# Kernel optimization log

Hardware: AMD Instinct MI355X
Metric: run time of the kernel (lower is better)

Reference implementation:

```python
import jax, jax.numpy as jnp
import numpy as np

HEADS = 8
DIM_HEAD = 32
DIM = HEADS * DIM_HEAD  # 256
B, H, W = 2, 256, 256


def _dw2d(x, wgt):
    # depthwise 3x3 conv, NCHW, weight (C,1,3,3)
    return jax.lax.conv_general_dilated(
        x, wgt, window_strides=(1, 1), padding='SAME',
        feature_group_count=x.shape[1],
        dimension_numbers=('NCHW', 'OIHW', 'NCHW'))


def setup_inputs() -> dict:
    key = jax.random.key(0)
    ks = jax.random.split(key, 20)
    def kaiming(k, shape, fan_in):
        return jax.random.normal(k, shape, jnp.float32) * np.sqrt(2.0 / fan_in)
    inp = {}
    inp['x_in'] = jax.random.normal(ks[0], (B, H, W, DIM), jnp.float32)
    # shared depthwise weights (heads,1,3,3), kaiming_normal fan_in=9
    names = ['qw1', 'qw2', 'qw3', 'kw1', 'kw2', 'kw3', 'vw1', 'vw2', 'vw3']
    for i, n in enumerate(names):
        inp[n] = kaiming(ks[1 + i], (HEADS, 1, 3, 3), 9)
    # pos_emb: two depthwise convs dim->dim with bias
    inp['pos_w1'] = kaiming(ks[10], (DIM, 1, 3, 3), 9)
    inp['pos_b1'] = jnp.zeros((DIM,), jnp.float32)
    inp['pos_w2'] = kaiming(ks[11], (DIM, 1, 3, 3), 9)
    inp['pos_b2'] = jnp.zeros((DIM,), jnp.float32)
    # conv1d heads->heads kernel 3
    inp['conv1d_w'] = kaiming(ks[12], (HEADS, HEADS, 3), HEADS * 3)
    inp['conv1d_b'] = jnp.zeros((HEADS,), jnp.float32)
    inp['rescale'] = jnp.ones((HEADS, 1, 1), jnp.float32)
    inp['rescale2'] = jnp.ones((HEADS, 1, 1), jnp.float32)
    inp['proj_w'] = kaiming(ks[13], (DIM, DIM), DIM)  # (out,in) torch layout
    inp['proj_b'] = jnp.zeros((DIM,), jnp.float32)
    return inp


def reference(x_in, qw1, qw2, qw3, kw1, kw2, kw3, vw1, vw2, vw3,
              pos_w1, pos_b1, pos_w2, pos_b2, conv1d_w, conv1d_b,
              rescale, rescale2, proj_w, proj_b):
    b, h, w, c = x_in.shape
    heads = rescale.shape[0]
    dim_head = c // heads
    x = jnp.transpose(x_in, (0, 3, 1, 2))  # NCHW
    # positional embedding: dwconv -> gelu(exact) -> dwconv
    t = _dw2d(x, pos_w1) + pos_b1[None, :, None, None]
    t = jax.nn.gelu(t, approximate=False)
    t = _dw2d(t, pos_w2) + pos_b2[None, :, None, None]
    x = x + t

    def chain(x, w1, w2, w3):
        for wgt in (w1, w2, w3):
            x = _dw2d(x, jnp.repeat(wgt, dim_head, axis=0))
        return x

    q = chain(x, qw1, qw2, qw3)
    k = chain(x, kw1, kw2, kw3)
    v = chain(x, vw1, vw2, vw3)
    # (b,c,h,w) -> (b,heads,dim_head,hw) ; channel = head*dim_head + d
    q = q.reshape(b, heads, dim_head, h * w)
    k = k.reshape(b, heads, dim_head, h * w)
    v = v.reshape(b, heads, dim_head, h * w)
    eps = 1e-12
    q = q / jnp.maximum(jnp.linalg.norm(q, axis=-1, keepdims=True), eps)
    k = k / jnp.maximum(jnp.linalg.norm(k, axis=-1, keepdims=True), eps)
    # channel attention: k @ q^T -> (b,heads,dim_head,dim_head)
    attn = jnp.einsum('bhdn,bhen->bhde', k, q)
    # pooled v -> conv1d over dim_head length, channels = heads
    y = v.mean(axis=-1)  # (b,heads,dim_head)
    attn_v = jax.lax.conv_general_dilated(
        y, conv1d_w, window_strides=(1,), padding='SAME',
        dimension_numbers=('NCH', 'OIH', 'NCH')) + conv1d_b[None, :, None]
    diag = attn_v[..., :, None] * jnp.eye(dim_head, dtype=attn.dtype)
    attn = attn * rescale[None] + diag * rescale2[None]
    attn = jax.nn.softmax(attn, axis=-1)
    out = jnp.einsum('bhde,bhen->bhdn', attn, v)  # (b,heads,dim_head,hw)
    out = jnp.transpose(out, (0, 3, 1, 2)).reshape(b, h * w, c)
    out = out @ proj_w.T + proj_b
    return out.reshape(b, h, w, c)
```

## Files before the change

### kernel.cpp

```cpp
#include <hip/hip_runtime.h>
#include <stdint.h>
#include <math.h>


using u16 = unsigned short;
using u32 = unsigned int;

typedef __bf16 bf16x8_t __attribute__((ext_vector_type(8)));
typedef float f32x4_t __attribute__((ext_vector_type(4)));

__device__ __forceinline__ float bf2f(u16 v) {
  u32 u = ((u32)v) << 16;
  return __builtin_bit_cast(float, u);
}
__device__ __forceinline__ u16 f2bf(float f) {
  u32 u = __builtin_bit_cast(u32, f);
  u32 r = u + 0x7fffu + ((u >> 16) & 1u);
  return (u16)(r >> 16);
}
__device__ __forceinline__ void unpack8(uint4 u, float f[8]) {
  f[0] = bf2f((u16)(u.x & 0xffffu)); f[1] = bf2f((u16)(u.x >> 16));
  f[2] = bf2f((u16)(u.y & 0xffffu)); f[3] = bf2f((u16)(u.y >> 16));
  f[4] = bf2f((u16)(u.z & 0xffffu)); f[5] = bf2f((u16)(u.z >> 16));
  f[6] = bf2f((u16)(u.w & 0xffffu)); f[7] = bf2f((u16)(u.w >> 16));
}
__device__ __forceinline__ uint4 pack8(const u16 o[8]) {
  uint4 v;
  v.x = (u32)o[0] | ((u32)o[1] << 16);
  v.y = (u32)o[2] | ((u32)o[3] << 16);
  v.z = (u32)o[4] | ((u32)o[5] << 16);
  v.w = (u32)o[6] | ((u32)o[7] << 16);
  return v;
}

__global__ __launch_bounds__(64) void compose_kernel(
    const float* __restrict__ qw1, const float* __restrict__ qw2,
    const float* __restrict__ qw3, const float* __restrict__ kw1,
    const float* __restrict__ kw2, const float* __restrict__ kw3,
    const float* __restrict__ vw1, const float* __restrict__ vw2,
    const float* __restrict__ vw3, float* __restrict__ Wc) {
  const int t = threadIdx.x;
  if (t >= 24) return;
  const int h = t / 3, c = t % 3;
  const float* w1 = (c == 0 ? qw1 : c == 1 ? kw1 : vw1) + h * 9;
  const float* w2 = (c == 0 ? qw2 : c == 1 ? kw2 : vw2) + h * 9;
  const float* w3 = (c == 0 ? qw3 : c == 1 ? kw3 : vw3) + h * 9;
  float w12[25];
  for (int i = 0; i < 25; ++i) w12[i] = 0.f;
  for (int ky = 0; ky < 3; ++ky)
    for (int kx = 0; kx < 3; ++kx)
      for (int ly = 0; ly < 3; ++ly)
        for (int lx = 0; lx < 3; ++lx)
          w12[(ky + ly) * 5 + kx + lx] += w2[ky * 3 + kx] * w1[ly * 3 + lx];
  float we[49];
  for (int i = 0; i < 49; ++i) we[i] = 0.f;
  for (int my = 0; my < 3; ++my)
    for (int mx = 0; mx < 3; ++mx)
      for (int ey = 0; ey < 5; ++ey)
        for (int ex = 0; ex < 5; ++ex)
          we[(my + ey) * 7 + mx + ex] += w3[my * 3 + mx] * w12[ey * 5 + ex];
  float* dst = Wc + (h * 3 + c) * 49;
  for (int i = 0; i < 49; ++i) dst[i] = we[i];
}

__global__ __launch_bounds__(256) void posemb_kernel(
    const float* __restrict__ xin, u16* __restrict__ x2,
    const float* __restrict__ w1g, const float* __restrict__ b1g,
    const float* __restrict__ w2g, const float* __restrict__ b2g) {
  const int t = threadIdx.x;
  const int o = t & 3;
  const int bz = blockIdx.z;
  const int cg = bz & 7;
  const int b = bz >> 3;
  const int x0 = blockIdx.x * 16;
  const int y0 = blockIdx.y * 8;
  const int c0 = cg * 32 + o * 8;

  __shared__ __align__(16) u16 Abuf[240 * 32];
  __shared__ __align__(16) u16 Bbuf[180 * 32];

  for (int i = t; i < 240 * 4; i += 256) {
    const int px = i >> 2, oo = i & 3;
    const int lx = px % 20, ly = px / 20;
    const int gx = x0 - 2 + lx, gy = y0 - 2 + ly;
    u16 ov[8];
    if (gx >= 0 && gx < 256 && gy >= 0 && gy < 256) {
      const float* p = xin + ((size_t)((b << 16) + (gy << 8) + gx)) * 256 + cg * 32 + oo * 8;
      const float4 r0 = *reinterpret_cast<const float4*>(p);
      const float4 r1 = *reinterpret_cast<const float4*>(p + 4);
      ov[0] = f2bf(r0.x); ov[1] = f2bf(r0.y); ov[2] = f2bf(r0.z); ov[3] = f2bf(r0.w);
      ov[4] = f2bf(r1.x); ov[5] = f2bf(r1.y); ov[6] = f2bf(r1.z); ov[7] = f2bf(r1.w);
    } else {
#pragma unroll
      for (int j = 0; j < 8; ++j) ov[j] = 0;
    }
    *reinterpret_cast<uint4*>(Abuf + px * 32 + oo * 8) = pack8(ov);
  }
  __syncthreads();

  {
    float w[72], bi[8];
#pragma unroll
    for (int j = 0; j < 8; ++j) {
#pragma unroll
      for (int k = 0; k < 9; ++k) w[j * 9 + k] = w1g[(c0 + j) * 9 + k];
      bi[j] = b1g[c0 + j];
    }
    for (int i = t; i < 180 * 4; i += 256) {
      const int px = i >> 2;
      const int sx = px % 18, sy = px / 18;
      const int gx = x0 - 1 + sx, gy = y0 - 1 + sy;
      const bool inb = (gx >= 0 && gx < 256 && gy >= 0 && gy < 256);
      float a[8];
#pragma unroll
      for (int j = 0; j < 8; ++j) a[j] = bi[j];
#pragma unroll
      for (int ky = 0; ky < 3; ++ky)
#pragma unroll
        for (int kx = 0; kx < 3; ++kx) {
          float f[8];
          unpack8(*reinterpret_cast<const uint4*>(
                      Abuf + ((sy + ky) * 20 + sx + kx) * 32 + o * 8), f);
#pragma unroll
          for (int j = 0; j < 8; ++j) a[j] = fmaf(w[j * 9 + ky * 3 + kx], f[j], a[j]);
        }
      u16 ov[8];
#pragma unroll
      for (int j = 0; j < 8; ++j) {
        const float g = 0.5f * a[j] * (1.0f + erff(a[j] * 0.70710678118654752f));
        ov[j] = inb ? f2bf(g) : (u16)0;
      }
      *reinterpret_cast<uint4*>(Bbuf + px * 32 + o * 8) = pack8(ov);
    }
  }
  __syncthreads();

  {
    float w[72], bi[8];
#pragma unroll
    for (int j = 0; j < 8; ++j) {
#pragma unroll
      for (int k = 0; k < 9; ++k) w[j * 9 + k] = w2g[(c0 + j) * 9 + k];
      bi[j] = b2g[c0 + j];
    }
    for (int i = t; i < 128 * 4; i += 256) {
      const int px = i >> 2;
      const int sx = px & 15, sy = px >> 4;
      float a[8];
#pragma unroll
      for (int j = 0; j < 8; ++j) a[j] = bi[j];
#pragma unroll
      for (int ky = 0; ky < 3; ++ky)
#pragma unroll
        for (int kx = 0; kx < 3; ++kx) {
          float f[8];
          unpack8(*reinterpret_cast<const uint4*>(
                      Bbuf + ((sy + ky) * 18 + sx + kx) * 32 + o * 8), f);
#pragma unroll
          for (int j = 0; j < 8; ++j) a[j] = fmaf(w[j * 9 + ky * 3 + kx], f[j], a[j]);
        }
      float xr[8];
      unpack8(*reinterpret_cast<const uint4*>(
                  Abuf + ((sy + 2) * 20 + sx + 2) * 32 + o * 8), xr);
      u16 ov[8];
#pragma unroll
      for (int j = 0; j < 8; ++j) ov[j] = f2bf(a[j] + xr[j]);
      u16* dst = x2 + ((size_t)((b << 16) + ((y0 + sy) << 8) + x0 + sx)) * 256 + cg * 32 + o * 8;
      *reinterpret_cast<uint4*>(dst) = pack8(ov);
    }
  }
}

__global__ __launch_bounds__(256) void qkv_fused_kernel(
    const u16* __restrict__ x2, u16* __restrict__ v3out,
    const float* __restrict__ Wc, float* __restrict__ G,
    float* __restrict__ sqq, float* __restrict__ sqk,
    float* __restrict__ vsum) {
  const int t = threadIdx.x;
  const int o = t & 3;
  const int sx = (t >> 2) & 15;
  const int yg = t >> 6;
  const int bz = blockIdx.z;
  const int h = bz & 7;
  const int b = bz >> 3;
  const int x0 = (blockIdx.x + 1) * 16;
  const int y0 = (blockIdx.y + 1) * 8;

  __shared__ __align__(16) u16 Abuf[308 * 32];
  __shared__ float rbuf[96];
  if (t < 96) rbuf[t] = 0.f;

  for (int i = t; i < 308 * 4; i += 256) {
    const int px = i >> 2, oo = i & 3;
    const int lx = px % 22, ly = px / 22;
    const int gx = x0 - 3 + lx, gy = y0 - 3 + ly;
    *reinterpret_cast<uint4*>(Abuf + px * 32 + oo * 8) =
        *reinterpret_cast<const uint4*>(
            x2 + ((size_t)((b << 16) + (gy << 8) + gx)) * 256 + h * 32 + oo * 8);
  }
  __syncthreads();

  const float* Wq = Wc + (h * 3 + 0) * 49;
  const float* Wk = Wc + (h * 3 + 1) * 49;
  const float* Wv = Wc + (h * 3 + 2) * 49;

  float aq[2][8], ak[2][8], av2[2][8];
#pragma unroll
  for (int r = 0; r < 2; ++r)
#pragma unroll
    for (int j = 0; j < 8; ++j) { aq[r][j] = 0.f; ak[r][j] = 0.f; av2[r][j] = 0.f; }

  const int ty0 = yg * 2;
  const u16* Arow0 = Abuf + (ty0 * 22 + sx) * 32 + o * 8;

  {
    const u16* Ar = Arow0;
#pragma unroll
    for (int jx = 0; jx < 7; ++jx) {
      float f[8];
      unpack8(*reinterpret_cast<const uint4*>(Ar + jx * 32), f);
      const float wq = Wq[jx], wk = Wk[jx], wv = Wv[jx];
#pragma unroll
      for (int j = 0; j < 8; ++j) {
        aq[0][j] = fmaf(wq, f[j], aq[0][j]);
        ak[0][j] = fmaf(wk, f[j], ak[0][j]);
        av2[0][j] = fmaf(wv, f[j], av2[0][j]);
      }
    }
  }
#pragma unroll 1
  for (int iy = 1; iy <= 6; ++iy) {
    const u16* Ar = Arow0 + iy * (22 * 32);
    const float* wq0 = Wq + iy * 7;
    const float* wk0 = Wk + iy * 7;
    const float* wv0 = Wv + iy * 7;
#pragma unroll
    for (int jx = 0; jx < 7; ++jx) {
      float f[8];
      unpack8(*reinterpret_cast<const uint4*>(Ar + jx * 32), f);
      float w;
      w = wq0[jx];
#pragma unroll
      for (int j = 0; j < 8; ++j) aq[0][j] = fmaf(w, f[j], aq[0][j]);
      w = wq0[jx - 7];
#pragma unroll
      for (int j = 0; j < 8; ++j) aq[1][j] = fmaf(w, f[j], aq[1][j]);
      w = wk0[jx];
#pragma unroll
      for (int j = 0; j < 8; ++j) ak[0][j] = fmaf(w, f[j], ak[0][j]);
      w = wk0[jx - 7];
#pragma unroll
      for (int j = 0; j < 8; ++j) ak[1][j] = fmaf(w, f[j], ak[1][j]);
      w = wv0[jx];
#pragma unroll
      for (int j = 0; j < 8; ++j) av2[0][j] = fmaf(w, f[j], av2[0][j]);
      w = wv0[jx - 7];
#pragma unroll
      for (int j = 0; j < 8; ++j) av2[1][j] = fmaf(w, f[j], av2[1][j]);
    }
  }
  {
    const u16* Ar = Arow0 + 7 * (22 * 32);
#pragma unroll
    for (int jx = 0; jx < 7; ++jx) {
      float f[8];
      unpack8(*reinterpret_cast<const uint4*>(Ar + jx * 32), f);
      const float wq = Wq[42 + jx], wk = Wk[42 + jx], wv = Wv[42 + jx];
#pragma unroll
      for (int j = 0; j < 8; ++j) {
        aq[1][j] = fmaf(wq, f[j], aq[1][j]);
        ak[1][j] = fmaf(wk, f[j], ak[1][j]);
        av2[1][j] = fmaf(wv, f[j], av2[1][j]);
      }
    }
  }

  __syncthreads();

  u16* K3s = Abuf;
  u16* Q3s = Abuf + 32 * 132;

  float rq[8], rk[8], rv[8];
#pragma unroll
  for (int j = 0; j < 8; ++j) { rq[j] = 0.f; rk[j] = 0.f; rv[j] = 0.f; }
#pragma unroll
  for (int ry = 0; ry < 2; ++ry) {
    const int px = (ty0 + ry) * 16 + sx;
    u16 ov[8];
#pragma unroll
    for (int j = 0; j < 8; ++j) {
      const u16 qb = f2bf(aq[ry][j]);
      Q3s[(o * 8 + j) * 132 + px] = qb;
      const float qf = bf2f(qb);
      rq[j] = fmaf(qf, qf, rq[j]);
      const u16 kb = f2bf(ak[ry][j]);
      K3s[(o * 8 + j) * 132 + px] = kb;
      const float kf = bf2f(kb);
      rk[j] = fmaf(kf, kf, rk[j]);
      ov[j] = f2bf(av2[ry][j]);
      rv[j] += bf2f(ov[j]);
    }
    u16* dst = v3out + ((size_t)((b << 16) + ((y0 + ty0 + ry) << 8) + x0 + sx)) * 256 + h * 32 + o * 8;
    *reinterpret_cast<uint4*>(dst) = pack8(ov);
  }
#pragma unroll
  for (int j = 0; j < 8; ++j) {
    atomicAdd(&rbuf[o * 8 + j], rq[j]);
    atomicAdd(&rbuf[32 + o * 8 + j], rk[j]);
    atomicAdd(&rbuf[64 + o * 8 + j], rv[j]);
  }
  __syncthreads();

  const int wave = t >> 6;
  const int lane = t & 63;
  const int quad = lane >> 4;
  const int l15 = lane & 15;
  const int d0 = (wave & 1) * 16;
  const int e0 = (wave >> 1) * 16;
  f32x4_t acc = {0.f, 0.f, 0.f, 0.f};
#pragma unroll
  for (int kb = 0; kb < 4; ++kb) {
    const bf16x8_t avf = *reinterpret_cast<const bf16x8_t*>(
        &K3s[(d0 + l15) * 132 + kb * 32 + quad * 8]);
    const bf16x8_t bvf = *reinterpret_cast<const bf16x8_t*>(
        &Q3s[(e0 + l15) * 132 + kb * 32 + quad * 8]);
    acc = __builtin_amdgcn_mfma_f32_16x16x32_bf16(avf, bvf, acc, 0, 0, 0);
  }
  float* Gp = G + (size_t)((b * 8 + h) * 32) * 32;
#pragma unroll
  for (int r = 0; r < 4; ++r)
    atomicAdd(&Gp[(d0 + quad * 4 + r) * 32 + e0 + l15], acc[r]);

  if (t < 32) atomicAdd(&sqq[b * 256 + h * 32 + t], rbuf[t]);
  else if (t < 64) atomicAdd(&sqk[b * 256 + h * 32 + (t - 32)], rbuf[t]);
  else if (t < 96) atomicAdd(&vsum[b * 256 + h * 32 + (t - 64)], rbuf[t]);
}

__device__ __forceinline__ void border_map(int bi, int& bx, int& by) {
  if (bi < 16) { bx = bi; by = 0; }
  else if (bi < 32) { bx = bi - 16; by = 31; }
  else { const int e = bi - 32; by = 1 + (e >> 1); bx = (e & 1) * 15; }
}

template <int RED, int BORDER>
__global__ __launch_bounds__(256) void chain3_kernel(
    const u16* __restrict__ in, u16* __restrict__ out,
    const float* __restrict__ w1g, const float* __restrict__ w2g,
    const float* __restrict__ w3g, float* __restrict__ red) {
  const int t = threadIdx.x;
  const int o = t & 3;
  const int bz = blockIdx.z;
  const int h = bz & 7;
  const int b = bz >> 3;
  int bx = blockIdx.x, by = blockIdx.y;
  if (BORDER) border_map(blockIdx.x, bx, by);
  const int x0 = bx * 16;
  const int y0 = by * 8;

  __shared__ __align__(16) u16 Abuf[308 * 32];
  __shared__ __align__(16) u16 Bbuf[240 * 32];
  __shared__ float rbuf[32];
  if (t < 32) rbuf[t] = 0.f;

  float w1[9], w2[9], w3[9];
#pragma unroll
  for (int k = 0; k < 9; ++k) {
    w1[k] = w1g[h * 9 + k];
    w2[k] = w2g[h * 9 + k];
    w3[k] = w3g[h * 9 + k];
  }

  for (int i = t; i < 308 * 4; i += 256) {
    const int px = i >> 2, oo = i & 3;
    const int lx = px % 22, ly = px / 22;
    const int gx = x0 - 3 + lx, gy = y0 - 3 + ly;
    uint4 v = {0, 0, 0, 0};
    if (gx >= 0 && gx < 256 && gy >= 0 && gy < 256)
      v = *reinterpret_cast<const uint4*>(
          in + ((size_t)((b << 16) + (gy << 8) + gx)) * 256 + h * 32 + oo * 8);
    *reinterpret_cast<uint4*>(Abuf + px * 32 + oo * 8) = v;
  }
  __syncthreads();

  for (int i = t; i < 240 * 4; i += 256) {
    const int px = i >> 2;
    const int sx = px % 20, sy = px / 20;
    const int gx = x0 - 2 + sx, gy = y0 - 2 + sy;
    const bool inb = (gx >= 0 && gx < 256 && gy >= 0 && gy < 256);
    float a[8] = {0, 0, 0, 0, 0, 0, 0, 0};
#pragma unroll
    for (int ky = 0; ky < 3; ++ky)
#pragma unroll
      for (int kx = 0; kx < 3; ++kx) {
        float f[8];
        unpack8(*reinterpret_cast<const uint4*>(
                    Abuf + ((sy + ky) * 22 + sx + kx) * 32 + o * 8), f);
#pragma unroll
        for (int j = 0; j < 8; ++j) a[j] = fmaf(w1[ky * 3 + kx], f[j], a[j]);
      }
    u16 ov[8];
#pragma unroll
    for (int j = 0; j < 8; ++j) ov[j] = inb ? f2bf(a[j]) : (u16)0;
    *reinterpret_cast<uint4*>(Bbuf + px * 32 + o * 8) = pack8(ov);
  }
  __syncthreads();

  for (int i = t; i < 180 * 4; i += 256) {
    const int px = i >> 2;
    const int sx = px % 18, sy = px / 18;
    const int gx = x0 - 1 + sx, gy = y0 - 1 + sy;
    const bool inb = (gx >= 0 && gx < 256 && gy >= 0 && gy < 256);
    float a[8] = {0, 0, 0, 0, 0, 0, 0, 0};
#pragma unroll
    for (int ky = 0; ky < 3; ++ky)
#pragma unroll
      for (int kx = 0; kx < 3; ++kx) {
        float f[8];
        unpack8(*reinterpret_cast<const uint4*>(
                    Bbuf + ((sy + ky) * 20 + sx + kx) * 32 + o * 8), f);
#pragma unroll
        for (int j = 0; j < 8; ++j) a[j] = fmaf(w2[ky * 3 + kx], f[j], a[j]);
      }
    u16 ov[8];
#pragma unroll
    for (int j = 0; j < 8; ++j) ov[j] = inb ? f2bf(a[j]) : (u16)0;
    *reinterpret_cast<uint4*>(Abuf + px * 32 + o * 8) = pack8(ov);
  }
  __syncthreads();

  float racc[8] = {0, 0, 0, 0, 0, 0, 0, 0};
  for (int i = t; i < 128 * 4; i += 256) {
    const int px = i >> 2;
    const int sx = px & 15, sy = px >> 4;
    float a[8] = {0, 0, 0, 0, 0, 0, 0, 0};
#pragma unroll
    for (int ky = 0; ky < 3; ++ky)
#pragma unroll
      for (int kx = 0; kx < 3; ++kx) {
        float f[8];
        unpack8(*reinterpret_cast<const uint4*>(
                    Abuf + ((sy + ky) * 18 + sx + kx) * 32 + o * 8), f);
#pragma unroll
        for (int j = 0; j < 8; ++j) a[j] = fmaf(w3[ky * 3 + kx], f[j], a[j]);
      }
    u16 ov[8];
#pragma unroll
    for (int j = 0; j < 8; ++j) {
      ov[j] = f2bf(a[j]);
      const float rv = bf2f(ov[j]);
      if (RED == 1) racc[j] = fmaf(rv, rv, racc[j]);
      if (RED == 2) racc[j] += rv;
    }
    u16* dst = out + ((size_t)((b << 16) + ((y0 + sy) << 8) + x0 + sx)) * 256 + h * 32 + o * 8;
    *reinterpret_cast<uint4*>(dst) = pack8(ov);
  }
  __syncthreads();
#pragma unroll
  for (int j = 0; j < 8; ++j) atomicAdd(&rbuf[o * 8 + j], racc[j]);
  __syncthreads();
  if (t < 32) atomicAdd(&red[b * 256 + h * 32 + t], rbuf[t]);
}

template <int BORDER>
__global__ __launch_bounds__(256) void kchain_gram_kernel(
    const u16* __restrict__ in, const u16* __restrict__ q3,
    const float* __restrict__ w1g, const float* __restrict__ w2g,
    const float* __restrict__ w3g, float* __restrict__ G, float* __restrict__ sqk) {
  const int t = threadIdx.x;
  const int o = t & 3;
  const int bz = blockIdx.z;
  const int h = bz & 7;
  const int b = bz >> 3;
  int bx = blockIdx.x, by = blockIdx.y;
  if (BORDER) border_map(blockIdx.x, bx, by);
  const int x0 = bx * 16;
  const int y0 = by * 8;

  __shared__ __align__(16) u16 Abuf[308 * 32];
  __shared__ __align__(16) u16 Bbuf[240 * 32];
  __shared__ __align__(16) u16 K3s[32 * 132];
  __shared__ __align__(16) u16 Q3s[32 * 132];
  __shared__ float rbuf[32];
  if (t < 32) rbuf[t] = 0.f;

  float w1[9], w2[9], w3[9];
#pragma unroll
  for (int k = 0; k < 9; ++k) {
    w1[k] = w1g[h * 9 + k];
    w2[k] = w2g[h * 9 + k];
    w3[k] = w3g[h * 9 + k];
  }

  for (int i = t; i < 308 * 4; i += 256) {
    const int px = i >> 2, oo = i & 3;
    const int lx = px % 22, ly = px / 22;
    const int gx = x0 - 3 + lx, gy = y0 - 3 + ly;
    uint4 v = {0, 0, 0, 0};
    if (gx >= 0 && gx < 256 && gy >= 0 && gy < 256)
      v = *reinterpret_cast<const uint4*>(
          in + ((size_t)((b << 16) + (gy << 8) + gx)) * 256 + h * 32 + oo * 8);
    *reinterpret_cast<uint4*>(Abuf + px * 32 + oo * 8) = v;
  }
  __syncthreads();

  for (int i = t; i < 240 * 4; i += 256) {
    const int px = i >> 2;
    const int sx = px % 20, sy = px / 20;
    const int gx = x0 - 2 + sx, gy = y0 - 2 + sy;
    const bool inb = (gx >= 0 && gx < 256 && gy >= 0 && gy < 256);
    float a[8] = {0, 0, 0, 0, 0, 0, 0, 0};
#pragma unroll
    for (int ky = 0; ky < 3; ++ky)
#pragma unroll
      for (int kx = 0; kx < 3; ++kx) {
        float f[8];
        unpack8(*reinterpret_cast<const uint4*>(
                    Abuf + ((sy + ky) * 22 + sx + kx) * 32 + o * 8), f);
#pragma unroll
        for (int j = 0; j < 8; ++j) a[j] = fmaf(w1[ky * 3 + kx], f[j], a[j]);
      }
    u16 ov[8];
#pragma unroll
    for (int j = 0; j < 8; ++j) ov[j] = inb ? f2bf(a[j]) : (u16)0;
    *reinterpret_cast<uint4*>(Bbuf + px * 32 + o * 8) = pack8(ov);
  }
  __syncthreads();

  for (int i = t; i < 180 * 4; i += 256) {
    const int px = i >> 2;
    const int sx = px % 18, sy = px / 18;
    const int gx = x0 - 1 + sx, gy = y0 - 1 + sy;
    const bool inb = (gx >= 0 && gx < 256 && gy >= 0 && gy < 256);
    float a[8] = {0, 0, 0, 0, 0, 0, 0, 0};
#pragma unroll
    for (int ky = 0; ky < 3; ++ky)
#pragma unroll
      for (int kx = 0; kx < 3; ++kx) {
        float f[8];
        unpack8(*reinterpret_cast<const uint4*>(
                    Bbuf + ((sy + ky) * 20 + sx + kx) * 32 + o * 8), f);
#pragma unroll
        for (int j = 0; j < 8; ++j) a[j] = fmaf(w2[ky * 3 + kx], f[j], a[j]);
      }
    u16 ov[8];
#pragma unroll
    for (int j = 0; j < 8; ++j) ov[j] = inb ? f2bf(a[j]) : (u16)0;
    *reinterpret_cast<uint4*>(Abuf + px * 32 + o * 8) = pack8(ov);
  }
  __syncthreads();

  float racc[8] = {0, 0, 0, 0, 0, 0, 0, 0};
  for (int i = t; i < 128 * 4; i += 256) {
    const int px = i >> 2;
    const int sx = px & 15, sy = px >> 4;
    float a[8] = {0, 0, 0, 0, 0, 0, 0, 0};
#pragma unroll
    for (int ky = 0; ky < 3; ++ky)
#pragma unroll
      for (int kx = 0; kx < 3; ++kx) {
        float f[8];
        unpack8(*reinterpret_cast<const uint4*>(
                    Abuf + ((sy + ky) * 18 + sx + kx) * 32 + o * 8), f);
#pragma unroll
        for (int j = 0; j < 8; ++j) a[j] = fmaf(w3[ky * 3 + kx], f[j], a[j]);
      }
#pragma unroll
    for (int j = 0; j < 8; ++j) {
      const u16 kb16 = f2bf(a[j]);
      const float kv = bf2f(kb16);
      K3s[(o * 8 + j) * 132 + px] = kb16;
      racc[j] = fmaf(kv, kv, racc[j]);
    }
    const uint4 uq = *reinterpret_cast<const uint4*>(
        q3 + ((size_t)((b << 16) + ((y0 + sy) << 8) + x0 + sx)) * 256 + h * 32 + o * 8);
    Q3s[(o * 8 + 0) * 132 + px] = (u16)(uq.x & 0xffffu);
    Q3s[(o * 8 + 1) * 132 + px] = (u16)(uq.x >> 16);
    Q3s[(o * 8 + 2) * 132 + px] = (u16)(uq.y & 0xffffu);
    Q3s[(o * 8 + 3) * 132 + px] = (u16)(uq.y >> 16);
    Q3s[(o * 8 + 4) * 132 + px] = (u16)(uq.z & 0xffffu);
    Q3s[(o * 8 + 5) * 132 + px] = (u16)(uq.z >> 16);
    Q3s[(o * 8 + 6) * 132 + px] = (u16)(uq.w & 0xffffu);
    Q3s[(o * 8 + 7) * 132 + px] = (u16)(uq.w >> 16);
  }
  __syncthreads();
#pragma unroll
  for (int j = 0; j < 8; ++j) atomicAdd(&rbuf[o * 8 + j], racc[j]);
  __syncthreads();
  if (t < 32) atomicAdd(&sqk[b * 256 + h * 32 + t], rbuf[t]);

  const int wave = t >> 6;
  const int lane = t & 63;
  const int quad = lane >> 4;
  const int l15 = lane & 15;
  const int d0 = (wave & 1) * 16;
  const int e0 = (wave >> 1) * 16;
  f32x4_t acc = {0.f, 0.f, 0.f, 0.f};
#pragma unroll
  for (int kb = 0; kb < 4; ++kb) {
    const bf16x8_t av = *reinterpret_cast<const bf16x8_t*>(
        &K3s[(d0 + l15) * 132 + kb * 32 + quad * 8]);
    const bf16x8_t bv = *reinterpret_cast<const bf16x8_t*>(
        &Q3s[(e0 + l15) * 132 + kb * 32 + quad * 8]);
    acc = __builtin_amdgcn_mfma_f32_16x16x32_bf16(av, bv, acc, 0, 0, 0);
  }
  float* Gp = G + (size_t)((b * 8 + h) * 32) * 32;
#pragma unroll
  for (int r = 0; r < 4; ++r)
    atomicAdd(&Gp[(d0 + quad * 4 + r) * 32 + e0 + l15], acc[r]);
}

__global__ __launch_bounds__(256) void attn_kernel(
    const float* __restrict__ G, const float* __restrict__ sqq,
    const float* __restrict__ sqk, const float* __restrict__ vsum,
    const float* __restrict__ cw, const float* __restrict__ cb,
    const float* __restrict__ rs1, const float* __restrict__ rs2,
    float* __restrict__ attn) {
  const int b = blockIdx.x;
  const int t = threadIdx.x;
  const int h = t >> 5;
  const int d = t & 31;
  __shared__ float vm[8][34];
  __shared__ float nq[256];
  vm[h][d + 1] = vsum[b * 256 + t] * (1.0f / 65536.0f);
  if (t < 8) { vm[t][0] = 0.f; vm[t][33] = 0.f; }
  nq[t] = fmaxf(sqrtf(sqq[b * 256 + t]), 1e-12f);
  __syncthreads();

  float av = cb[h];
#pragma unroll
  for (int i = 0; i < 8; ++i)
#pragma unroll
    for (int tau = 0; tau < 3; ++tau)
      av = fmaf(cw[h * 24 + i * 3 + tau], vm[i][d + tau], av);

  const float nk = fmaxf(sqrtf(sqk[b * 256 + t]), 1e-12f);
  const float rsc = rs1[h];
  const float rsc2 = rs2[h];
  const float* Gp = G + (size_t)((b * 8 + h) * 32 + d) * 32;
  float L[32];
#pragma unroll
  for (int e = 0; e < 32; ++e) {
    float l = Gp[e] * rsc / (nk * nq[h * 32 + e]);
    if (e == d) l += av * rsc2;
    L[e] = l;
  }
  float mx = L[0];
#pragma unroll
  for (int e = 1; e < 32; ++e) mx = fmaxf(mx, L[e]);
  float s = 0.f;
#pragma unroll
  for (int e = 0; e < 32; ++e) {
    L[e] = expf(L[e] - mx);
    s += L[e];
  }
  const float inv = 1.0f / s;
  float* Ap = attn + (size_t)((b * 8 + h) * 32 + d) * 32;
#pragma unroll
  for (int e = 0; e < 32; ++e) Ap[e] = L[e] * inv;
}

__global__ __launch_bounds__(256) void mbuild_kernel(
    const float* __restrict__ attn, const float* __restrict__ pw,
    u16* __restrict__ M) {
  const int bid = blockIdx.x;
  const int b = bid >> 3;
  const int h = bid & 7;
  const int t = threadIdx.x;
  __shared__ float at[32][33];
#pragma unroll
  for (int i = 0; i < 4; ++i) {
    const int idx = t * 4 + i;
    at[idx >> 5][idx & 31] = attn[(size_t)(b * 8 + h) * 1024 + idx];
  }
  __syncthreads();
  float pwf[32];
#pragma unroll
  for (int dd = 0; dd < 32; ++dd) pwf[dd] = pw[(size_t)t * 256 + h * 32 + dd];
  u16* Mp = M + (size_t)b * 65536 + (size_t)t * 256 + h * 32;
#pragma unroll
  for (int e = 0; e < 32; ++e) {
    float s = 0.f;
#pragma unroll
    for (int dd = 0; dd < 32; ++dd) s = fmaf(pwf[dd], at[dd][e], s);
    Mp[e] = f2bf(s);
  }
}

__global__ __launch_bounds__(256) void gemm_kernel(
    const u16* __restrict__ V, const u16* __restrict__ Mm,
    const float* __restrict__ pb, float* __restrict__ out) {
  const int m0 = blockIdx.x * 128;
  const int n0 = blockIdx.y * 64;
  const int b = m0 >> 16;
  const u16* Mb = Mm + (size_t)b * 65536;

  __shared__ __align__(16) u16 As[128][72];
  __shared__ __align__(16) u16 Bs[64][72];

  const int t = threadIdx.x;
  const int wave = t >> 6;
  const int lane = t & 63;
  const int quad = lane >> 4;
  const int l15 = lane & 15;

  f32x4_t acc[2][4];
#pragma unroll
  for (int mt = 0; mt < 2; ++mt)
#pragma unroll
    for (int nt = 0; nt < 4; ++nt) acc[mt][nt] = {0.f, 0.f, 0.f, 0.f};

  for (int k0 = 0; k0 < 256; k0 += 64) {
#pragma unroll
    for (int i = 0; i < 4; ++i) {
      const int id = t + 256 * i;
      const int row = id >> 3;
      const int c8 = id & 7;
      *reinterpret_cast<uint4*>(&As[row][c8 * 8]) = *reinterpret_cast<const uint4*>(
          &V[(size_t)(m0 + row) * 256 + k0 + c8 * 8]);
    }
#pragma unroll
    for (int i = 0; i < 2; ++i) {
      const int id = t + 256 * i;
      const int row = id >> 3;
      const int c8 = id & 7;
      *reinterpret_cast<uint4*>(&Bs[row][c8 * 8]) = *reinterpret_cast<const uint4*>(
          &Mb[(size_t)(n0 + row) * 256 + k0 + c8 * 8]);
    }
    __syncthreads();
#pragma unroll
    for (int ks = 0; ks < 2; ++ks) {
      bf16x8_t af[2], bfv[4];
#pragma unroll
      for (int mt = 0; mt < 2; ++mt)
        af[mt] = *reinterpret_cast<const bf16x8_t*>(
            &As[wave * 32 + mt * 16 + l15][ks * 32 + quad * 8]);
#pragma unroll
      for (int nt = 0; nt < 4; ++nt)
        bfv[nt] = *reinterpret_cast<const bf16x8_t*>(
            &Bs[nt * 16 + l15][ks * 32 + quad * 8]);
#pragma unroll
      for (int mt = 0; mt < 2; ++mt)
#pragma unroll
        for (int nt = 0; nt < 4; ++nt)
          acc[mt][nt] =
              __builtin_amdgcn_mfma_f32_16x16x32_bf16(af[mt], bfv[nt], acc[mt][nt], 0, 0, 0);
    }
    __syncthreads();
  }

#pragma unroll
  for (int nt = 0; nt < 4; ++nt) {
    const int col = n0 + nt * 16 + l15;
    const float pbf = pb[col];
#pragma unroll
    for (int mt = 0; mt < 2; ++mt) {
#pragma unroll
      for (int r = 0; r < 4; ++r) {
        const int m = m0 + wave * 32 + mt * 16 + quad * 4 + r;
        out[(size_t)m * 256 + col] = acc[mt][nt][r] + pbf;
      }
    }
  }
}

extern "C" void kernel_launch(void* const* d_in, const int* in_sizes, int n_in,
                              void* d_out, int out_size, void* d_ws, size_t ws_size,
                              hipStream_t stream) {
  const float* x_in = (const float*)d_in[0];
  const float* qw1 = (const float*)d_in[1];
  const float* qw2 = (const float*)d_in[2];
  const float* qw3 = (const float*)d_in[3];
  const float* kw1 = (const float*)d_in[4];
  const float* kw2 = (const float*)d_in[5];
  const float* kw3 = (const float*)d_in[6];
  const float* vw1 = (const float*)d_in[7];
  const float* vw2 = (const float*)d_in[8];
  const float* vw3 = (const float*)d_in[9];
  const float* posw1 = (const float*)d_in[10];
  const float* posb1 = (const float*)d_in[11];
  const float* posw2 = (const float*)d_in[12];
  const float* posb2 = (const float*)d_in[13];
  const float* cw = (const float*)d_in[14];
  const float* cb = (const float*)d_in[15];
  const float* rs1 = (const float*)d_in[16];
  const float* rs2 = (const float*)d_in[17];
  const float* pw = (const float*)d_in[18];
  const float* pb = (const float*)d_in[19];

  char* ws = (char*)d_ws;
  const size_t SLOT = 67108864;
  u16* S0 = (u16*)(ws);
  u16* S1 = (u16*)(ws + SLOT);
  u16* D0 = (u16*)d_out;
  char* SM = ws + 2 * SLOT;
  float* G = (float*)(SM);
  float* sqq = (float*)(SM + 65536);
  float* sqk = (float*)(SM + 67584);
  float* vsum = (float*)(SM + 69632);
  float* attn = (float*)(SM + 71680);
  u16* Mm = (u16*)(SM + 137216);
  float* Wc = (float*)(SM + 399360);

  hipMemsetAsync(SM, 0, 71680, stream);

  compose_kernel<<<1, 64, 0, stream>>>(qw1, qw2, qw3, kw1, kw2, kw3,
                                       vw1, vw2, vw3, Wc);

  const dim3 tgrid(16, 32, 16);
  posemb_kernel<<<tgrid, 256, 0, stream>>>(x_in, S0, posw1, posb1, posw2, posb2);

  qkv_fused_kernel<<<dim3(14, 30, 16), 256, 0, stream>>>(S0, S1, Wc, G, sqq, sqk, vsum);

  const dim3 bgrid(92, 1, 16);
  chain3_kernel<1, 1><<<bgrid, 256, 0, stream>>>(S0, D0, qw1, qw2, qw3, sqq);
  kchain_gram_kernel<1><<<bgrid, 256, 0, stream>>>(S0, D0, kw1, kw2, kw3, G, sqk);
  chain3_kernel<2, 1><<<bgrid, 256, 0, stream>>>(S0, S1, vw1, vw2, vw3, vsum);

  attn_kernel<<<2, 256, 0, stream>>>(G, sqq, sqk, vsum, cw, cb, rs1, rs2, attn);
  mbuild_kernel<<<16, 256, 0, stream>>>(attn, pw, Mm);
  gemm_kernel<<<dim3(1024, 4), 256, 0, stream>>>(S1, Mm, pb, (float*)d_out);
}
```

Baseline: 878.5 us.

## Fuse border-tile q/k/v chain and gram kernels into one launch

Replaces the three border-tile kernels (q chain, k chain with gram, v chain) with one kernel that loads the halo once and runs the three 3-conv chains in sequence. The q result stays in shared memory instead of going through global memory and being read back for the gram product. This removes two kernel launches, two redundant halo loads and the q3 round trip. In exchange, shared-memory use per block rises, because an extra Cbuf is added, and the three chains now run serially inside each block, which may lower occupancy.

After: 872.2 us. About the same (-0.7%).

```diff
diff --git a/kernel.cpp b/kernel.cpp
--- a/kernel.cpp
+++ b/kernel.cpp
@@ -342,33 +342,32 @@
   else { const int e = bi - 32; by = 1 + (e >> 1); bx = (e & 1) * 15; }
 }
 
-template <int RED, int BORDER>
-__global__ __launch_bounds__(256) void chain3_kernel(
-    const u16* __restrict__ in, u16* __restrict__ out,
-    const float* __restrict__ w1g, const float* __restrict__ w2g,
-    const float* __restrict__ w3g, float* __restrict__ red) {
+__global__ __launch_bounds__(256) void border_fused_kernel(
+    const u16* __restrict__ in, u16* __restrict__ v3out,
+    const float* __restrict__ qw1, const float* __restrict__ qw2,
+    const float* __restrict__ qw3, const float* __restrict__ kw1,
+    const float* __restrict__ kw2, const float* __restrict__ kw3,
+    const float* __restrict__ vw1, const float* __restrict__ vw2,
+    const float* __restrict__ vw3, float* __restrict__ G,
+    float* __restrict__ sqq, float* __restrict__ sqk,
+    float* __restrict__ vsum) {
   const int t = threadIdx.x;
   const int o = t & 3;
   const int bz = blockIdx.z;
   const int h = bz & 7;
   const int b = bz >> 3;
-  int bx = blockIdx.x, by = blockIdx.y;
-  if (BORDER) border_map(blockIdx.x, bx, by);
+  int bx, by;
+  border_map(blockIdx.x, bx, by);
   const int x0 = bx * 16;
   const int y0 = by * 8;
 
-  __shared__ __align__(16) u16 Abuf[308 * 32];
+  __shared__ __align__(16) u16 Halo[308 * 32];
   __shared__ __align__(16) u16 Bbuf[240 * 32];
-  __shared__ float rbuf[32];
-  if (t < 32) rbuf[t] = 0.f;
-
-  float w1[9], w2[9], w3[9];
-#pragma unroll
-  for (int k = 0; k < 9; ++k) {
-    w1[k] = w1g[h * 9 + k];
-    w2[k] = w2g[h * 9 + k];
-    w3[k] = w3g[h * 9 + k];
-  }
+  __shared__ __align__(16) u16 Cbuf[180 * 32];
+  __shared__ __align__(16) u16 K3s[32 * 132];
+  __shared__ __align__(16) u16 Q3s[32 * 132];
+  __shared__ float rbuf[96];
+  if (t < 96) rbuf[t] = 0.f;
 
   for (int i = t; i < 308 * 4; i += 256) {
     const int px = i >> 2, oo = i & 3;
@@ -378,215 +377,113 @@
     if (gx >= 0 && gx < 256 && gy >= 0 && gy < 256)
       v = *reinterpret_cast<const uint4*>(
           in + ((size_t)((b << 16) + (gy << 8) + gx)) * 256 + h * 32 + oo * 8);
-    *reinterpret_cast<uint4*>(Abuf + px * 32 + oo * 8) = v;
+    *reinterpret_cast<uint4*>(Halo + px * 32 + oo * 8) = v;
   }
   __syncthreads();
 
-  for (int i = t; i < 240 * 4; i += 256) {
-    const int px = i >> 2;
-    const int sx = px % 20, sy = px / 20;
-    const int gx = x0 - 2 + sx, gy = y0 - 2 + sy;
-    const bool inb = (gx >= 0 && gx < 256 && gy >= 0 && gy < 256);
-    float a[8] = {0, 0, 0, 0, 0, 0, 0, 0};
-#pragma unroll
-    for (int ky = 0; ky < 3; ++ky)
-#pragma unroll
-      for (int kx = 0; kx < 3; ++kx) {
-        float f[8];
-        unpack8(*reinterpret_cast<const uint4*>(
-                    Abuf + ((sy + ky) * 22 + sx + kx) * 32 + o * 8), f);
-#pragma unroll
-        for (int j = 0; j < 8; ++j) a[j] = fmaf(w1[ky * 3 + kx], f[j], a[j]);
+#pragma unroll 1
+  for (int c = 0; c < 3; ++c) {
+    const float* w1g = (c == 0 ? qw1 : c == 1 ? kw1 : vw1);
+    const float* w2g = (c == 0 ? qw2 : c == 1 ? kw2 : vw2);
+    const float* w3g = (c == 0 ? qw3 : c == 1 ? kw3 : vw3);
+    float w1[9], w2[9], w3[9];
+#pragma unroll
+    for (int k = 0; k < 9; ++k) {
+      w1[k] = w1g[h * 9 + k];
+      w2[k] = w2g[h * 9 + k];
+      w3[k] = w3g[h * 9 + k];
+    }
+
+    for (int i = t; i < 240 * 4; i += 256) {
+      const int px = i >> 2;
+      const int sx = px % 20, sy = px / 20;
+      const int gx = x0 - 2 + sx, gy = y0 - 2 + sy;
+      const bool inb = (gx >= 0 && gx < 256 && gy >= 0 && gy < 256);
+      float a[8] = {0, 0, 0, 0, 0, 0, 0, 0};
+#pragma unroll
+      for (int ky = 0; ky < 3; ++ky)
+#pragma unroll
+        for (int kx = 0; kx < 3; ++kx) {
+          float f[8];
+          unpack8(*reinterpret_cast<const uint4*>(
+                      Halo + ((sy + ky) * 22 + sx + kx) * 32 + o * 8), f);
+#pragma unroll
+          for (int j = 0; j < 8; ++j) a[j] = fmaf(w1[ky * 3 + kx], f[j], a[j]);
+        }
+      u16 ov[8];
+#pragma unroll
+      for (int j = 0; j < 8; ++j) ov[j] = inb ? f2bf(a[j]) : (u16)0;
+      *reinterpret_cast<uint4*>(Bbuf + px * 32 + o * 8) = pack8(ov);
+    }
+    __syncthreads();
+
+    for (int i = t; i < 180 * 4; i += 256) {
+      const int px = i >> 2;
+      const int sx = px % 18, sy = px / 18;
+      const int gx = x0 - 1 + sx, gy = y0 - 1 + sy;
+      const bool inb = (gx >= 0 && gx < 256 && gy >= 0 && gy < 256);
+      float a[8] = {0, 0, 0, 0, 0, 0, 0, 0};
+#pragma unroll
+      for (int ky = 0; ky < 3; ++ky)
+#pragma unroll
+        for (int kx = 0; kx < 3; ++kx) {
+          float f[8];
+          unpack8(*reinterpret_cast<const uint4*>(
+                      Bbuf + ((sy + ky) * 20 + sx + kx) * 32 + o * 8), f);
+#pragma unroll
+          for (int j = 0; j < 8; ++j) a[j] = fmaf(w2[ky * 3 + kx], f[j], a[j]);
+        }
+      u16 ov[8];
+#pragma unroll
+      for (int j = 0; j < 8; ++j) ov[j] = inb ? f2bf(a[j]) : (u16)0;
+      *reinterpret_cast<uint4*>(Cbuf + px * 32 + o * 8) = pack8(ov);
+    }
+    __syncthreads();
+
+    float racc[8] = {0, 0, 0, 0, 0, 0, 0, 0};
+    for (int i = t; i < 128 * 4; i += 256) {
+      const int px = i >> 2;
+      const int sx = px & 15, sy = px >> 4;
+      float a[8] = {0, 0, 0, 0, 0, 0, 0, 0};
+#pragma unroll
+      for (int ky = 0; ky < 3; ++ky)
+#pragma unroll
+        for (int kx = 0; kx < 3; ++kx) {
+          float f[8];
+          unpack8(*reinterpret_cast<const uint4*>(
+                      Cbuf + ((sy + ky) * 18 + sx + kx) * 32 + o * 8), f);
+#pragma unroll
+          for (int j = 0; j < 8; ++j) a[j] = fmaf(w3[ky * 3 + kx], f[j], a[j]);
+        }
+      u16 ov[8];
+#pragma unroll
+      for (int j = 0; j < 8; ++j) ov[j] = f2bf(a[j]);
+      if (c == 0) {
+#pragma unroll
+        for (int j = 0; j < 8; ++j) {
+          Q3s[(o * 8 + j) * 132 + px] = ov[j];
+          const float f = bf2f(ov[j]);
+          racc[j] = fmaf(f, f, racc[j]);
+        }
+      } else if (c == 1) {
+#pragma unroll
+        for (int j = 0; j < 8; ++j) {
+          K3s[(o * 8 + j) * 132 + px] = ov[j];
+          const float f = bf2f(ov[j]);
+          racc[j] = fmaf(f, f, racc[j]);
+        }
+      } else {
+#pragma unroll
+        for (int j = 0; j < 8; ++j) racc[j] += bf2f(ov[j]);
+        u16* dst = v3out + ((size_t)((b << 16) + ((y0 + sy) << 8) + x0 + sx)) * 256 + h * 32 + o * 8;
+        *reinterpret_cast<uint4*>(dst) = pack8(ov);
       }
-    u16 ov[8];
-#pragma unroll
-    for (int j = 0; j < 8; ++j) ov[j] = inb ? f2bf(a[j]) : (u16)0;
-    *reinterpret_cast<uint4*>(Bbuf + px * 32 + o * 8) = pack8(ov);
-  }
-  __syncthreads();
-
-  for (int i = t; i < 180 * 4; i += 256) {
-    const int px = i >> 2;
-    const int sx = px % 18, sy = px / 18;
-    const int gx = x0 - 1 + sx, gy = y0 - 1 + sy;
-    const bool inb = (gx >= 0 && gx < 256 && gy >= 0 && gy < 256);
-    float a[8] = {0, 0, 0, 0, 0, 0, 0, 0};
-#pragma unroll
-    for (int ky = 0; ky < 3; ++ky)
-#pragma unroll
-      for (int kx = 0; kx < 3; ++kx) {
-        float f[8];
-        unpack8(*reinterpret_cast<const uint4*>(
-                    Bbuf + ((sy + ky) * 20 + sx + kx) * 32 + o * 8), f);
-#pragma unroll
-        for (int j = 0; j < 8; ++j) a[j] = fmaf(w2[ky * 3 + kx], f[j], a[j]);
-      }
-    u16 ov[8];
-#pragma unroll
-    for (int j = 0; j < 8; ++j) ov[j] = inb ? f2bf(a[j]) : (u16)0;
-    *reinterpret_cast<uint4*>(Abuf + px * 32 + o * 8) = pack8(ov);
-  }
-  __syncthreads();
-
-  float racc[8] = {0, 0, 0, 0, 0, 0, 0, 0};
-  for (int i = t; i < 128 * 4; i += 256) {
-    const int px = i >> 2;
-    const int sx = px & 15, sy = px >> 4;
-    float a[8] = {0, 0, 0, 0, 0, 0, 0, 0};
-#pragma unroll
-    for (int ky = 0; ky < 3; ++ky)
-#pragma unroll
-      for (int kx = 0; kx < 3; ++kx) {
-        float f[8];
-        unpack8(*reinterpret_cast<const uint4*>(
-                    Abuf + ((sy + ky) * 18 + sx + kx) * 32 + o * 8), f);
-#pragma unroll
-        for (int j = 0; j < 8; ++j) a[j] = fmaf(w3[ky * 3 + kx], f[j], a[j]);
-      }
-    u16 ov[8];
-#pragma unroll
-    for (int j = 0; j < 8; ++j) {
-      ov[j] = f2bf(a[j]);
-      const float rv = bf2f(ov[j]);
-      if (RED == 1) racc[j] = fmaf(rv, rv, racc[j]);
-      if (RED == 2) racc[j] += rv;
-    }
-    u16* dst = out + ((size_t)((b << 16) + ((y0 + sy) << 8) + x0 + sx)) * 256 + h * 32 + o * 8;
-    *reinterpret_cast<uint4*>(dst) = pack8(ov);
-  }
-  __syncthreads();
-#pragma unroll
-  for (int j = 0; j < 8; ++j) atomicAdd(&rbuf[o * 8 + j], racc[j]);
-  __syncthreads();
-  if (t < 32) atomicAdd(&red[b * 256 + h * 32 + t], rbuf[t]);
-}
-
-template <int BORDER>
-__global__ __launch_bounds__(256) void kchain_gram_kernel(
-    const u16* __restrict__ in, const u16* __restrict__ q3,
-    const float* __restrict__ w1g, const float* __restrict__ w2g,
-    const float* __restrict__ w3g, float* __restrict__ G, float* __restrict__ sqk) {
-  const int t = threadIdx.x;
-  const int o = t & 3;
-  const int bz = blockIdx.z;
-  const int h = bz & 7;
-  const int b = bz >> 3;
-  int bx = blockIdx.x, by = blockIdx.y;
-  if (BORDER) border_map(blockIdx.x, bx, by);
-  const int x0 = bx * 16;
-  const int y0 = by * 8;
-
-  __shared__ __align__(16) u16 Abuf[308 * 32];
-  __shared__ __align__(16) u16 Bbuf[240 * 32];
-  __shared__ __align__(16) u16 K3s[32 * 132];
-  __shared__ __align__(16) u16 Q3s[32 * 132];
-  __shared__ float rbuf[32];
-  if (t < 32) rbuf[t] = 0.f;
-
-  float w1[9], w2[9], w3[9];
-#pragma unroll
-  for (int k = 0; k < 9; ++k) {
-    w1[k] = w1g[h * 9 + k];
-    w2[k] = w2g[h * 9 + k];
-    w3[k] = w3g[h * 9 + k];
-  }
-
-  for (int i = t; i < 308 * 4; i += 256) {
-    const int px = i >> 2, oo = i & 3;
-    const int lx = px % 22, ly = px / 22;
-    const int gx = x0 - 3 + lx, gy = y0 - 3 + ly;
-    uint4 v = {0, 0, 0, 0};
-    if (gx >= 0 && gx < 256 && gy >= 0 && gy < 256)
-      v = *reinterpret_cast<const uint4*>(
-          in + ((size_t)((b << 16) + (gy << 8) + gx)) * 256 + h * 32 + oo * 8);
-    *reinterpret_cast<uint4*>(Abuf + px * 32 + oo * 8) = v;
-  }
-  __syncthreads();
-
-  for (int i = t; i < 240 * 4; i += 256) {
-    const int px = i >> 2;
-    const int sx = px % 20, sy = px / 20;
-    const int gx = x0 - 2 + sx, gy = y0 - 2 + sy;
-    const bool inb = (gx >= 0 && gx < 256 && gy >= 0 && gy < 256);
-    float a[8] = {0, 0, 0, 0, 0, 0, 0, 0};
-#pragma unroll
-    for (int ky = 0; ky < 3; ++ky)
-#pragma unroll
-      for (int kx = 0; kx < 3; ++kx) {
-        float f[8];
-        unpack8(*reinterpret_cast<const uint4*>(
-                    Abuf + ((sy + ky) * 22 + sx + kx) * 32 + o * 8), f);
-#pragma unroll
-        for (int j = 0; j < 8; ++j) a[j] = fmaf(w1[ky * 3 + kx], f[j], a[j]);
-      }
-    u16 ov[8];
-#pragma unroll
-    for (int j = 0; j < 8; ++j) ov[j] = inb ? f2bf(a[j]) : (u16)0;
-    *reinterpret_cast<uint4*>(Bbuf + px * 32 + o * 8) = pack8(ov);
-  }
-  __syncthreads();
-
-  for (int i = t; i < 180 * 4; i += 256) {
-    const int px = i >> 2;
-    const int sx = px % 18, sy = px / 18;
-    const int gx = x0 - 1 + sx, gy = y0 - 1 + sy;
-    const bool inb = (gx >= 0 && gx < 256 && gy >= 0 && gy < 256);
-    float a[8] = {0, 0, 0, 0, 0, 0, 0, 0};
-#pragma unroll
-    for (int ky = 0; ky < 3; ++ky)
-#pragma unroll
-      for (int kx = 0; kx < 3; ++kx) {
-        float f[8];
-        unpack8(*reinterpret_cast<const uint4*>(
-                    Bbuf + ((sy + ky) * 20 + sx + kx) * 32 + o * 8), f);
-#pragma unroll
-        for (int j = 0; j < 8; ++j) a[j] = fmaf(w2[ky * 3 + kx], f[j], a[j]);
-      }
-    u16 ov[8];
-#pragma unroll
-    for (int j = 0; j < 8; ++j) ov[j] = inb ? f2bf(a[j]) : (u16)0;
-    *reinterpret_cast<uint4*>(Abuf + px * 32 + o * 8) = pack8(ov);
-  }
-  __syncthreads();
-
-  float racc[8] = {0, 0, 0, 0, 0, 0, 0, 0};
-  for (int i = t; i < 128 * 4; i += 256) {
-    const int px = i >> 2;
-    const int sx = px & 15, sy = px >> 4;
-    float a[8] = {0, 0, 0, 0, 0, 0, 0, 0};
-#pragma unroll
-    for (int ky = 0; ky < 3; ++ky)
-#pragma unroll
-      for (int kx = 0; kx < 3; ++kx) {
-        float f[8];
-        unpack8(*reinterpret_cast<const uint4*>(
-                    Abuf + ((sy + ky) * 18 + sx + kx) * 32 + o * 8), f);
-#pragma unroll
-        for (int j = 0; j < 8; ++j) a[j] = fmaf(w3[ky * 3 + kx], f[j], a[j]);
-      }
-#pragma unroll
-    for (int j = 0; j < 8; ++j) {
-      const u16 kb16 = f2bf(a[j]);
-      const float kv = bf2f(kb16);
-      K3s[(o * 8 + j) * 132 + px] = kb16;
-      racc[j] = fmaf(kv, kv, racc[j]);
-    }
-    const uint4 uq = *reinterpret_cast<const uint4*>(
-        q3 + ((size_t)((b << 16) + ((y0 + sy) << 8) + x0 + sx)) * 256 + h * 32 + o * 8);
-    Q3s[(o * 8 + 0) * 132 + px] = (u16)(uq.x & 0xffffu);
-    Q3s[(o * 8 + 1) * 132 + px] = (u16)(uq.x >> 16);
-    Q3s[(o * 8 + 2) * 132 + px] = (u16)(uq.y & 0xffffu);
-    Q3s[(o * 8 + 3) * 132 + px] = (u16)(uq.y >> 16);
-    Q3s[(o * 8 + 4) * 132 + px] = (u16)(uq.z & 0xffffu);
-    Q3s[(o * 8 + 5) * 132 + px] = (u16)(uq.z >> 16);
-    Q3s[(o * 8 + 6) * 132 + px] = (u16)(uq.w & 0xffffu);
-    Q3s[(o * 8 + 7) * 132 + px] = (u16)(uq.w >> 16);
-  }
-  __syncthreads();
-#pragma unroll
-  for (int j = 0; j < 8; ++j) atomicAdd(&rbuf[o * 8 + j], racc[j]);
-  __syncthreads();
-  if (t < 32) atomicAdd(&sqk[b * 256 + h * 32 + t], rbuf[t]);
+    }
+    __syncthreads();
+#pragma unroll
+    for (int j = 0; j < 8; ++j) atomicAdd(&rbuf[c * 32 + o * 8 + j], racc[j]);
+    __syncthreads();
+  }
 
   const int wave = t >> 6;
   const int lane = t & 63;
@@ -607,6 +504,10 @@
 #pragma unroll
   for (int r = 0; r < 4; ++r)
     atomicAdd(&Gp[(d0 + quad * 4 + r) * 32 + e0 + l15], acc[r]);
+
+  if (t < 32) atomicAdd(&sqq[b * 256 + h * 32 + t], rbuf[t]);
+  else if (t < 64) atomicAdd(&sqk[b * 256 + h * 32 + (t - 32)], rbuf[t]);
+  else if (t < 96) atomicAdd(&vsum[b * 256 + h * 32 + (t - 64)], rbuf[t]);
 }
 
 __global__ __launch_bounds__(256) void attn_kernel(
@@ -791,7 +692,6 @@
   const size_t SLOT = 67108864;
   u16* S0 = (u16*)(ws);
   u16* S1 = (u16*)(ws + SLOT);
-  u16* D0 = (u16*)d_out;
   char* SM = ws + 2 * SLOT;
   float* G = (float*)(SM);
   float* sqq = (float*)(SM + 65536);
@@ -811,10 +711,8 @@
 
   qkv_fused_kernel<<<dim3(14, 30, 16), 256, 0, stream>>>(S0, S1, Wc, G, sqq, sqk, vsum);
 
-  const dim3 bgrid(92, 1, 16);
-  chain3_kernel<1, 1><<<bgrid, 256, 0, stream>>>(S0, D0, qw1, qw2, qw3, sqq);
-  kchain_gram_kernel<1><<<bgrid, 256, 0, stream>>>(S0, D0, kw1, kw2, kw3, G, sqk);
-  chain3_kernel<2, 1><<<bgrid, 256, 0, stream>>>(S0, S1, vw1, vw2, vw3, vsum);
+  border_fused_kernel<<<dim3(92, 1, 16), 256, 0, stream>>>(
+      S0, S1, qw1, qw2, qw3, kw1, kw2, kw3, vw1, vw2, vw3, G, sqq, sqk, vsum);
 
   attn_kernel<<<2, 256, 0, stream>>>(G, sqq, sqk, vsum, cw, cb, rs1, rs2, attn);
   mbuild_kernel<<<16, 256, 0, stream>>>(attn, pw, Mm);
```
